# Performance work log

Measured on AMD Instinct MI355X. Metric: run time of the kernel, lower is better.

## Reference

```python
import jax, jax.numpy as jnp
import numpy as np

N = 50000
P = 200000
L = 6
IN_DIM = 128
OUT_DIM = 128
HEADS = 4


def setup_inputs() -> dict:
    key = jax.random.key(0)
    ks = jax.random.split(key, 7)
    x = jax.random.normal(ks[0], (N, IN_DIM), dtype=jnp.float32)
    path_list = jax.random.randint(ks[1], (P, L), 0, N, dtype=jnp.int64)
    s = 0.1
    w_ih = jax.random.normal(ks[2], (3 * OUT_DIM, IN_DIM), dtype=jnp.float32) * s
    w_hh = jax.random.normal(ks[3], (3 * OUT_DIM, OUT_DIM), dtype=jnp.float32) * s
    b_ih = jax.random.normal(ks[4], (3 * OUT_DIM,), dtype=jnp.float32) * s
    b_hh = jax.random.normal(ks[5], (3 * OUT_DIM,), dtype=jnp.float32) * s
    a = jax.random.uniform(ks[6], (OUT_DIM, HEADS), dtype=jnp.float32) * 2.0 - 1.0
    return {"x": x, "path_list": path_list, "w_ih": w_ih, "w_hh": w_hh,
            "b_ih": b_ih, "b_hh": b_hh, "a": a}


def _gru_final_hidden(feats, w_ih, w_hh, b_ih, b_hh):
    # feats: [P, L, in_dim]; PyTorch GRU cell semantics, h0 = 0.
    out_dim = w_hh.shape[1]
    p = feats.shape[0]

    def step(h, xt):
        gi = xt @ w_ih.T + b_ih          # [P, 3*out]
        gh = h @ w_hh.T + b_hh           # [P, 3*out]
        ir, iz, i_n = jnp.split(gi, 3, axis=-1)
        hr, hz, h_n = jnp.split(gh, 3, axis=-1)
        r = jax.nn.sigmoid(ir + hr)
        z = jax.nn.sigmoid(iz + hz)
        n_cand = jnp.tanh(i_n + r * h_n)
        h_new = (1.0 - z) * n_cand + z * h
        return h_new, None

    h0 = jnp.zeros((p, out_dim), feats.dtype)
    xs = jnp.swapaxes(feats, 0, 1)       # [L, P, in_dim]
    h, _ = jax.lax.scan(step, h0, xs)
    return h                              # [P, out_dim]


def reference(x, path_list, w_ih, w_hh, b_ih, b_hh, a):
    n, out_dim = x.shape[0], w_hh.shape[1]
    heads = a.shape[1]
    # F.embedding(path_list, x): gather path features [P, L, in_dim]
    feats = x[path_list]
    path_emb = _gru_final_hidden(feats, w_ih, w_hh, b_ih, b_hh)       # [P, out]
    # unnormalized attention per head
    att_un = jnp.exp(jax.nn.leaky_relu(path_emb @ a, negative_slope=0.2))  # [P, H]
    row = path_list[:, -1]                                             # owner node of each path
    # M @ att_un : segment-sum over owner nodes
    att_sum = jax.ops.segment_sum(att_un, row, num_segments=n)         # [N, H]
    # M.t() @ (1/att_sum) : gather back to paths
    att_low = (1.0 / att_sum)[row]                                     # [P, H]
    att_n = att_un * att_low                                           # [P, H]
    # reshape(-1,1).repeat(1,out).reshape(P,-1): each head's scalar repeated out_dim times
    att_rep = jnp.repeat(att_n, out_dim, axis=1)                       # [P, H*out]
    emb_rep = jnp.tile(path_emb, (1, heads))                           # [P, H*out]
    path_att_emb = att_rep * emb_rep
    node_att_emb = jax.ops.segment_sum(path_att_emb, row, num_segments=n)  # [N, H*out]
    return node_att_emb
```

## Files before the change

kernel.cpp:

```cpp
#include <hip/hip_runtime.h>
#include <hip/hip_bf16.h>
#include <math.h>

#define NN 50000
#define PP 200000
#define LL 6
#define DD 128
#define HH 4

#define TM 64
#define NT 512
#define HPAD 132

typedef __attribute__((ext_vector_type(8))) short short8;
typedef __attribute__((ext_vector_type(4))) float f32x4;

__device__ __forceinline__ unsigned short f2bf(float v) {
    __hip_bfloat16 h = __float2bfloat16(v);
    return *(unsigned short*)&h;
}
__device__ __forceinline__ float bf2f(unsigned short u) {
    union { unsigned int i; float f; } c; c.i = ((unsigned int)u) << 16; return c.f;
}
__device__ __forceinline__ unsigned short f2h(float v) {
    _Float16 h = (_Float16)v;
    return *(unsigned short*)&h;
}
__device__ __forceinline__ float h2f(unsigned short u) {
    _Float16 h = *(_Float16*)&u;
    return (float)h;
}
__device__ __forceinline__ float fast_rcp(float x) { return __builtin_amdgcn_rcpf(x); }
__device__ __forceinline__ float fast_sigmoid(float x) {
    return fast_rcp(1.f + __expf(-x));
}
__device__ __forceinline__ float fast_tanh(float x) {
    float e = __expf(-2.f * fabsf(x));
    float t = (1.f - e) * fast_rcp(1.f + e);
    return copysignf(t, x);
}

__global__ void prep_w_kernel(const float* __restrict__ w_hh,
                              unsigned short* __restrict__ whb) {
    int i = blockIdx.x * 256 + threadIdx.x;
    if (i < 3 * DD * DD) whb[i] = f2bf(w_hh[i]);
}

__global__ void histo_kernel(const int* __restrict__ path_list,
                             int* __restrict__ cnt) {
    int p = blockIdx.x * 256 + threadIdx.x;
    if (p < PP) atomicAdd(&cnt[path_list[p * LL + (LL - 1)]], 1);
}

__global__ void scan_kernel(const int* __restrict__ cnt,
                            int* __restrict__ offs,
                            int* __restrict__ cursor) {
    __shared__ int ls[256];
    const int t = threadIdx.x;
    const int chunk = (NN + 255) / 256;
    int s = 0;
    for (int j = 0; j < chunk; ++j) {
        int i = t + j * 256;
        if (i < NN) s += cnt[i];
    }
    ls[t] = s; __syncthreads();
    for (int off = 1; off < 256; off <<= 1) {
        int v = (t >= off) ? ls[t - off] : 0;
        __syncthreads();
        ls[t] += v;
        __syncthreads();
    }
    int run = (t == 0) ? 0 : ls[t - 1];
    for (int j = 0; j < chunk; ++j) {
        int i = t + j * 256;
        if (i < NN) { offs[i] = run; cursor[i] = run; run += cnt[i]; }
    }
}

__global__ void scatter_kernel(const int* __restrict__ path_list,
                               int* __restrict__ cursor,
                               int* __restrict__ sorted) {
    int p = blockIdx.x * 256 + threadIdx.x;
    if (p < PP) {
        int row = path_list[p * LL + (LL - 1)];
        int k = atomicAdd(&cursor[row], 1);
        sorted[k] = p;
    }
}

__global__ __launch_bounds__(512, 2)
void gi_gemm_kernel(const float* __restrict__ x,
                    const float* __restrict__ w_ih,
                    const float* __restrict__ b_ih,
                    const float* __restrict__ b_hh,
                    unsigned int*   __restrict__ giRZ,
                    unsigned short* __restrict__ giN)
{
    const int tid  = threadIdx.x;
    const int lane = tid & 63;
    const int wave = tid >> 6;
    const int lcol = lane & 15;
    const int quad = lane >> 4;
    const int ko   = quad * 8;
    const int d    = wave * 16 + lcol;
    const int r0   = blockIdx.x * 64;

    short8 B[3][4];
    float bias[3];
    #pragma unroll
    for (int c = 0; c < 3; ++c) {
        int col = c * 128 + d;
        #pragma unroll
        for (int ks = 0; ks < 4; ++ks) {
            const float4* src = (const float4*)(w_ih + (size_t)col * 128 + ks * 32 + ko);
            float4 f0 = src[0], f1 = src[1];
            short8 b;
            b[0] = (short)f2bf(f0.x); b[1] = (short)f2bf(f0.y);
            b[2] = (short)f2bf(f0.z); b[3] = (short)f2bf(f0.w);
            b[4] = (short)f2bf(f1.x); b[5] = (short)f2bf(f1.y);
            b[6] = (short)f2bf(f1.z); b[7] = (short)f2bf(f1.w);
            B[c][ks] = b;
        }
        bias[c] = b_ih[col] + ((c < 2) ? b_hh[col] : 0.f);
    }

    f32x4 acc[3][4];
    #pragma unroll
    for (int c = 0; c < 3; ++c)
        #pragma unroll
        for (int rt = 0; rt < 4; ++rt)
            acc[c][rt] = (f32x4){bias[c], bias[c], bias[c], bias[c]};

    #pragma unroll
    for (int ks = 0; ks < 4; ++ks) {
        #pragma unroll
        for (int rt = 0; rt < 4; ++rt) {
            int row = r0 + rt * 16 + lcol;
            if (row >= NN) row = NN - 1;
            const float4* src = (const float4*)(x + (size_t)row * 128 + ks * 32 + ko);
            float4 f0 = src[0], f1 = src[1];
            short8 av;
            av[0] = (short)f2bf(f0.x); av[1] = (short)f2bf(f0.y);
            av[2] = (short)f2bf(f0.z); av[3] = (short)f2bf(f0.w);
            av[4] = (short)f2bf(f1.x); av[5] = (short)f2bf(f1.y);
            av[6] = (short)f2bf(f1.z); av[7] = (short)f2bf(f1.w);
            acc[0][rt] = __builtin_amdgcn_mfma_f32_16x16x32_bf16(av, B[0][ks], acc[0][rt], 0, 0, 0);
            acc[1][rt] = __builtin_amdgcn_mfma_f32_16x16x32_bf16(av, B[1][ks], acc[1][rt], 0, 0, 0);
            acc[2][rt] = __builtin_amdgcn_mfma_f32_16x16x32_bf16(av, B[2][ks], acc[2][rt], 0, 0, 0);
        }
    }

    #pragma unroll
    for (int rt = 0; rt < 4; ++rt)
        #pragma unroll
        for (int rr = 0; rr < 4; ++rr) {
            int row = r0 + rt * 16 + quad * 4 + rr;
            if (row < NN) {
                unsigned int rz = (unsigned int)f2h(acc[0][rt][rr])
                                | ((unsigned int)f2h(acc[1][rt][rr]) << 16);
                giRZ[(size_t)row * 128 + d] = rz;
                giN [(size_t)row * 128 + d] = f2h(acc[2][rt][rr]);
            }
        }
}

__global__ __launch_bounds__(NT, 2)
void gru_att_kernel(const unsigned int*   __restrict__ giRZ,
                    const unsigned short* __restrict__ giN,
                    const int*   __restrict__ path_list,
                    const unsigned short* __restrict__ whb,
                    const float* __restrict__ b_hh,
                    const float* __restrict__ a,
                    float* __restrict__ att_sum,
                    unsigned short* __restrict__ emb,
                    float* __restrict__ att_un_g)
{
    __shared__ __align__(16) unsigned char smem[43520];
    unsigned short* hs0    = (unsigned short*)smem;
    unsigned short* hs1    = (unsigned short*)(smem + 16384);
    float*          hs_f   = (float*)smem;
    float*          red_s  = (float*)(smem + 33792);
    int*            nodes_s= (int*)(smem + 41984);

    const int tid  = threadIdx.x;
    const int lane = tid & 63;
    const int wave = tid >> 6;
    const int lcol = lane & 15;
    const int quad = lane >> 4;
    const int d    = wave * 16 + lcol;
    const int p0   = blockIdx.x * TM;
    const int ko   = quad * 8;

    short8 Bh[3][4];
    #pragma unroll
    for (int c = 0; c < 3; ++c)
        #pragma unroll
        for (int ks = 0; ks < 4; ++ks)
            Bh[c][ks] = *(const short8*)(whb + (size_t)(c * DD + d) * DD + ks * 32 + ko);
    const float bhn = b_hh[d + 256];

    for (int i = tid; i < TM * LL; i += NT) nodes_s[i] = path_list[(size_t)p0 * LL + i];
    for (int i = tid; i < TM * DD / 8; i += NT)
        ((uint4*)hs0)[i] = make_uint4(0u, 0u, 0u, 0u);

    float hreg[16];
    #pragma unroll
    for (int i = 0; i < 16; ++i) hreg[i] = 0.f;

    __syncthreads();

    #pragma unroll 1
    for (int t = 0; t < LL; ++t) {
        unsigned short* hr = (t & 1) ? hs1 : hs0;
        unsigned short* hw = (t & 1) ? hs0 : hs1;

        float gin[16];
        f32x4 accR[4], accZ[4], accH[4];
        #pragma unroll
        for (int rt = 0; rt < 4; ++rt)
            #pragma unroll
            for (int r = 0; r < 4; ++r) {
                const int p = rt * 16 + quad * 4 + r;
                const int node = nodes_s[p * LL + t];
                unsigned int rz   = giRZ[(size_t)node * 128 + d];
                unsigned short nn = giN [(size_t)node * 128 + d];
                accR[rt][r] = h2f((unsigned short)(rz & 0xffffu));
                accZ[rt][r] = h2f((unsigned short)(rz >> 16));
                gin[rt * 4 + r] = h2f(nn);
            }
        #pragma unroll
        for (int rt = 0; rt < 4; ++rt)
            accH[rt] = (f32x4){bhn, bhn, bhn, bhn};

        #pragma unroll
        for (int ks = 0; ks < 4; ++ks) {
            const int kb = ks * 4 + quad;
            #pragma unroll
            for (int rt = 0; rt < 4; ++rt) {
                const int p = rt * 16 + lcol;
                short8 ah = *(const short8*)(hr + p * DD + ((kb ^ lcol) * 8));
                accR[rt] = __builtin_amdgcn_mfma_f32_16x16x32_bf16(ah, Bh[0][ks], accR[rt], 0, 0, 0);
                accZ[rt] = __builtin_amdgcn_mfma_f32_16x16x32_bf16(ah, Bh[1][ks], accZ[rt], 0, 0, 0);
                accH[rt] = __builtin_amdgcn_mfma_f32_16x16x32_bf16(ah, Bh[2][ks], accH[rt], 0, 0, 0);
            }
        }

        if (t == LL - 1) __syncthreads();

        #pragma unroll
        for (int rt = 0; rt < 4; ++rt) {
            #pragma unroll
            for (int r = 0; r < 4; ++r) {
                const int idx = rt * 4 + r;
                const int p   = rt * 16 + quad * 4 + r;
                float rg = fast_sigmoid(accR[rt][r]);
                float zg = fast_sigmoid(accZ[rt][r]);
                float ng = fast_tanh(gin[idx] + rg * accH[rt][r]);
                float hnew = fmaf(zg, hreg[idx] - ng, ng);
                hreg[idx] = hnew;
                if (t < LL - 1) {
                    hw[p * DD + (((d >> 3) ^ (p & 15)) * 8) + (d & 7)] = f2bf(hnew);
                } else {
                    hs_f[p * HPAD + d] = hnew;
                }
            }
        }
        __syncthreads();
    }

    {
        int pi = tid >> 3, tt = tid & 7;
        float s0 = 0.f, s1 = 0.f, s2 = 0.f, s3 = 0.f;
        unsigned short pack[16];
        #pragma unroll
        for (int j = 0; j < 16; ++j) {
            int dd2 = tt * 16 + j;
            float hv = hs_f[pi * HPAD + dd2];
            pack[j] = f2bf(hv);
            float4 av = *(const float4*)(a + dd2 * 4);
            s0 += hv * av.x; s1 += hv * av.y; s2 += hv * av.z; s3 += hv * av.w;
        }
        uint4* dst = (uint4*)(emb + (size_t)(p0 + pi) * DD + tt * 16);
        dst[0] = *(uint4*)&pack[0];
        dst[1] = *(uint4*)&pack[8];
        float* rp = red_s + (pi * 8 + tt) * 4;
        rp[0] = s0; rp[1] = s1; rp[2] = s2; rp[3] = s3;
    }
    __syncthreads();
    if (tid < TM) {
        int pi = tid;
        int row = nodes_s[pi * LL + (LL - 1)];
        float4 e4;
        #pragma unroll
        for (int h = 0; h < HH; ++h) {
            float s = 0.f;
            #pragma unroll
            for (int tt = 0; tt < 8; ++tt) s += red_s[(pi * 8 + tt) * 4 + h];
            float lv = (s > 0.f) ? s : 0.2f * s;
            float e  = __expf(lv);
            ((float*)&e4)[h] = e;
            atomicAdd(&att_sum[row * HH + h], e);
        }
        *(float4*)(att_un_g + (size_t)(p0 + pi) * HH) = e4;
    }
}

__global__ __launch_bounds__(256)
void agg_kernel(const unsigned short* __restrict__ emb,
                const float* __restrict__ att_un,
                const float* __restrict__ att_sum,
                const int* __restrict__ offs,
                const int* __restrict__ cnt,
                const int* __restrict__ sorted,
                float* __restrict__ out)
{
    int node = blockIdx.x * 2 + (threadIdx.x >> 7);
    int d    = threadIdx.x & 127;
    if (node >= NN) return;
    int start = offs[node];
    int len   = cnt[node];
    float a0 = 0.f, a1 = 0.f, a2 = 0.f, a3 = 0.f;
    for (int i = 0; i < len; ++i) {
        int p = sorted[start + i];
        float4 at = *(const float4*)(att_un + (size_t)p * 4);
        float ev = bf2f(emb[(size_t)p * DD + d]);
        a0 = fmaf(at.x, ev, a0);
        a1 = fmaf(at.y, ev, a1);
        a2 = fmaf(at.z, ev, a2);
        a3 = fmaf(at.w, ev, a3);
    }
    float4 s = *(const float4*)(att_sum + (size_t)node * 4);
    float* o = out + (size_t)node * 512 + d;
    o[0]   = (s.x > 0.f) ? a0 / s.x : 0.f;
    o[128] = (s.y > 0.f) ? a1 / s.y : 0.f;
    o[256] = (s.z > 0.f) ? a2 / s.z : 0.f;
    o[384] = (s.w > 0.f) ? a3 / s.w : 0.f;
}

extern "C" void kernel_launch(void* const* d_in, const int* in_sizes, int n_in,
                              void* d_out, int out_size, void* d_ws, size_t ws_size,
                              hipStream_t stream) {
    const float* x         = (const float*)d_in[0];
    const int*   path_list = (const int*)  d_in[1];
    const float* w_ih      = (const float*)d_in[2];
    const float* w_hh      = (const float*)d_in[3];
    const float* b_ih      = (const float*)d_in[4];
    const float* b_hh      = (const float*)d_in[5];
    const float* a         = (const float*)d_in[6];
    float* out = (float*)d_out;

    char* w = (char*)d_ws;
    float*          att_sum = (float*)w;                 w += 800000;
    int*            cnt     = (int*)w;                   w += 200000;
    int*            offs    = (int*)w;                   w += 200000;
    int*            cursor  = (int*)w;                   w += 200000;
    int*            sorted  = (int*)w;                   w += 800000;
    float*          att_un  = (float*)w;                 w += 3200000;
    unsigned int*   giRZ    = (unsigned int*)w;          w += 25600000;
    unsigned short* giN     = (unsigned short*)w;        w += 12800000;
    unsigned short* whb     = (unsigned short*)w;        w += 98304;
    unsigned short* emb     = (unsigned short*)w;        w += 51200000;

    hipMemsetAsync(att_sum, 0, 800000, stream);
    hipMemsetAsync(cnt, 0, 200000, stream);

    prep_w_kernel<<<(3 * DD * DD + 255) / 256, 256, 0, stream>>>(w_hh, whb);

    histo_kernel<<<(PP + 255) / 256, 256, 0, stream>>>(path_list, cnt);
    scan_kernel<<<1, 256, 0, stream>>>(cnt, offs, cursor);
    scatter_kernel<<<(PP + 255) / 256, 256, 0, stream>>>(path_list, cursor, sorted);

    gi_gemm_kernel<<<(NN + 63) / 64, 512, 0, stream>>>(x, w_ih, b_ih, b_hh, giRZ, giN);

    gru_att_kernel<<<PP / TM, NT, 0, stream>>>(giRZ, giN, path_list, whb,
                                               b_hh, a, att_sum, emb, att_un);

    agg_kernel<<<(NN + 1) / 2, 256, 0, stream>>>(emb, att_un, att_sum,
                                                 offs, cnt, sorted, out);
}
```

Measured before the change: 736.8 us.

## Prefetch gathered GRU input-gate rows into LDS with double-buffered async loads

The GRU kernel used to gather the per-step input-gate values (giRZ, giN) directly from global memory inside the recurrence loop. They are now loaded with global_load_lds into double-buffered padded LDS tiles, so step t+1 is fetched while step t computes. Each step's gate values are then read from LDS. This hides the latency of the random gathers, but LDS per block grows from about 43KB to about 144KB. That likely cuts residency to one block per CU and relies on correct waits and barriers around the asynchronous LDS writes.

```diff
diff --git a/kernel.cpp b/kernel.cpp
--- a/kernel.cpp
+++ b/kernel.cpp
@@ -38,6 +38,12 @@
     float e = __expf(-2.f * fabsf(x));
     float t = (1.f - e) * fast_rcp(1.f + e);
     return copysignf(t, x);
+}
+
+__device__ __forceinline__ void gload_lds4(const unsigned int* g, unsigned int* l) {
+    __builtin_amdgcn_global_load_lds(
+        (const __attribute__((address_space(1))) unsigned int*)g,
+        (__attribute__((address_space(3))) unsigned int*)l, 4, 0, 0);
 }
 
 __global__ void prep_w_kernel(const float* __restrict__ w_hh,
@@ -165,8 +171,8 @@
 }
 
 __global__ __launch_bounds__(NT, 2)
-void gru_att_kernel(const unsigned int*   __restrict__ giRZ,
-                    const unsigned short* __restrict__ giN,
+void gru_att_kernel(const unsigned int* __restrict__ giRZ,
+                    const unsigned int* __restrict__ giN32,
                     const int*   __restrict__ path_list,
                     const unsigned short* __restrict__ whb,
                     const float* __restrict__ b_hh,
@@ -175,12 +181,16 @@
                     unsigned short* __restrict__ emb,
                     float* __restrict__ att_un_g)
 {
-    __shared__ __align__(16) unsigned char smem[43520];
+    __shared__ __align__(16) unsigned char smem[143872];
     unsigned short* hs0    = (unsigned short*)smem;
     unsigned short* hs1    = (unsigned short*)(smem + 16384);
+    unsigned int*   gz0    = (unsigned int*)(smem + 32768);
+    unsigned int*   gz1    = (unsigned int*)(smem + 66560);
+    unsigned int*   gn0    = (unsigned int*)(smem + 100352);
+    unsigned int*   gn1    = (unsigned int*)(smem + 117248);
     float*          hs_f   = (float*)smem;
-    float*          red_s  = (float*)(smem + 33792);
-    int*            nodes_s= (int*)(smem + 41984);
+    float*          red_s  = (float*)(smem + 134144);
+    int*            nodes_s= (int*)(smem + 142336);
 
     const int tid  = threadIdx.x;
     const int lane = tid & 63;
@@ -200,6 +210,29 @@
     const float bhn = b_hh[d + 256];
 
     for (int i = tid; i < TM * LL; i += NT) nodes_s[i] = path_list[(size_t)p0 * LL + i];
+    __syncthreads();
+
+    #define STAGE_GI(gz, gn, tt)                                              \
+        {                                                                     \
+            _Pragma("unroll")                                                 \
+            for (int j = 0; j < 16; ++j) {                                    \
+                int hr_ = wave * 16 + j;                                      \
+                int pp_ = hr_ >> 1, hf_ = hr_ & 1;                            \
+                int nd_ = nodes_s[pp_ * LL + (tt)];                           \
+                gload_lds4(giRZ + (size_t)nd_ * 128 + hf_ * 64 + lane,        \
+                           (gz) + pp_ * 132 + hf_ * 64);                      \
+            }                                                                 \
+            _Pragma("unroll")                                                 \
+            for (int j = 0; j < 8; ++j) {                                     \
+                int pp_ = wave * 8 + j;                                       \
+                int nd_ = nodes_s[pp_ * LL + (tt)];                           \
+                gload_lds4(giN32 + (size_t)nd_ * 64 + lane,                   \
+                           (gn) + pp_ * 66);                                  \
+            }                                                                 \
+        }
+
+    STAGE_GI(gz0, gn0, 0);
+
     for (int i = tid; i < TM * DD / 8; i += NT)
         ((uint4*)hs0)[i] = make_uint4(0u, 0u, 0u, 0u);
 
@@ -213,24 +246,29 @@
     for (int t = 0; t < LL; ++t) {
         unsigned short* hr = (t & 1) ? hs1 : hs0;
         unsigned short* hw = (t & 1) ? hs0 : hs1;
+        unsigned int*   gzc = (t & 1) ? gz1 : gz0;
+        unsigned int*   gnc = (t & 1) ? gn1 : gn0;
+
+        if (t < LL - 1) {
+            if (t & 1) { STAGE_GI(gz0, gn0, t + 1); }
+            else       { STAGE_GI(gz1, gn1, t + 1); }
+        }
 
         float gin[16];
         f32x4 accR[4], accZ[4], accH[4];
         #pragma unroll
-        for (int rt = 0; rt < 4; ++rt)
+        for (int rt = 0; rt < 4; ++rt) {
             #pragma unroll
             for (int r = 0; r < 4; ++r) {
                 const int p = rt * 16 + quad * 4 + r;
-                const int node = nodes_s[p * LL + t];
-                unsigned int rz   = giRZ[(size_t)node * 128 + d];
-                unsigned short nn = giN [(size_t)node * 128 + d];
+                unsigned int rz   = gzc[p * 132 + d];
+                unsigned short nn = ((const unsigned short*)gnc)[p * 132 + d];
                 accR[rt][r] = h2f((unsigned short)(rz & 0xffffu));
                 accZ[rt][r] = h2f((unsigned short)(rz >> 16));
                 gin[rt * 4 + r] = h2f(nn);
             }
-        #pragma unroll
-        for (int rt = 0; rt < 4; ++rt)
             accH[rt] = (f32x4){bhn, bhn, bhn, bhn};
+        }
 
         #pragma unroll
         for (int ks = 0; ks < 4; ++ks) {
@@ -303,6 +341,7 @@
         }
         *(float4*)(att_un_g + (size_t)(p0 + pi) * HH) = e4;
     }
+    #undef STAGE_GI
 }
 
 __global__ __launch_bounds__(256)
@@ -372,7 +411,8 @@
 
     gi_gemm_kernel<<<(NN + 63) / 64, 512, 0, stream>>>(x, w_ih, b_ih, b_hh, giRZ, giN);
 
-    gru_att_kernel<<<PP / TM, NT, 0, stream>>>(giRZ, giN, path_list, whb,
+    gru_att_kernel<<<PP / TM, NT, 0, stream>>>(giRZ, (const unsigned int*)giN,
+                                               path_list, whb,
                                                b_hh, a, att_sum, emb, att_un);
 
     agg_kernel<<<(NN + 1) / 2, 256, 0, stream>>>(emb, att_un, att_sum,
```

Result: no change. 723.1 us (-1.9%).
